# Performance work log

Measured on AMD Instinct MI355X. Metric: run time of the kernel, lower is better.

The kernel has to match this reference:

```python
import jax, jax.numpy as jnp
import numpy as np

B, N, C = 4, 4096, 128  # batch, tokens (flattened 3D volume), channels
F = 128  # filters


def setup_inputs() -> dict:
    key = jax.random.key(0)
    ks = jax.random.split(key, 7)
    s = 1.0 / np.sqrt(C)
    return {
        "inputs": jax.random.normal(ks[0], (B, N, C), dtype=jnp.float32),
        "Wq": jax.random.normal(ks[1], (C, F), dtype=jnp.float32) * s,
        "bq": jnp.zeros((F,), dtype=jnp.float32),
        "Wk": jax.random.normal(ks[2], (C, F), dtype=jnp.float32) * s,
        "bk": jnp.zeros((F,), dtype=jnp.float32),
        "Wv": jax.random.normal(ks[3], (C, F), dtype=jnp.float32) * s,
        "bv": jnp.zeros((F,), dtype=jnp.float32),
    }


def reference(inputs, Wq, bq, Wk, bk, Wv, bv):
    # Dense projections
    q = inputs @ Wq + bq  # [B, N, F]
    k = inputs @ Wk + bk
    v = inputs @ Wv + bv
    scale = jnp.sqrt(jnp.asarray(F, dtype=q.dtype))
    scores = jnp.einsum("bnf,bmf->bnm", q, k) / scale  # [B, N, N]
    weights = jax.nn.softmax(scores, axis=-1)
    return jnp.einsum("bnm,bmf->bnf", weights, v)
```

## Files before the change

### kernel.cpp

```cpp
#include <hip/hip_runtime.h>

typedef unsigned short u16;
typedef unsigned int u32;
typedef float f32x4 __attribute__((ext_vector_type(4)));
typedef short s16x8 __attribute__((ext_vector_type(8)));
typedef unsigned int u32x2 __attribute__((ext_vector_type(2)));
typedef unsigned int u32x4 __attribute__((ext_vector_type(4)));

#define NB 4
#define NT 4096
#define ND 128
#define NQ (NB * NT)

#define QK_SCALE 0.12751879523138906f

using as3_void = __attribute__((address_space(3))) void;
using as1_void = __attribute__((address_space(1))) void;

__device__ __forceinline__ u16 f2bf(float x){
  unsigned u = __float_as_uint(x);
  return (u16)((u + 0x7FFFu + ((u >> 16) & 1u)) >> 16);
}
__device__ __forceinline__ u32 cvtpk(float lo, float hi){
  u32 r; asm("v_cvt_pk_bf16_f32 %0, %1, %2" : "=v"(r) : "v"(lo), "v"(hi)); return r;
}
__device__ __forceinline__ f32x4 mfma16(s16x8 a, s16x8 b, f32x4 c){
  return __builtin_amdgcn_mfma_f32_16x16x32_bf16(a, b, c, 0, 0, 0);
}

__global__ void k_wprep(const float* __restrict__ Wq, const float* __restrict__ Wk,
                        const float* __restrict__ Wv, u16* __restrict__ WT){
  int mat = blockIdx.x >> 7;
  int f   = blockIdx.x & 127;
  const float* W = (mat == 0) ? Wq : (mat == 1) ? Wk : Wv;
  int c = threadIdx.x;
  WT[mat * 16384 + f * 128 + c] = f2bf(W[c * 128 + f]);
}

__global__ __launch_bounds__(256) void k_proj(
    const float* __restrict__ X, const u16* __restrict__ WT,
    const float* __restrict__ bq, const float* __restrict__ bk, const float* __restrict__ bv,
    u16* __restrict__ Qs, u16* __restrict__ Ks, u16* __restrict__ VTs)
{
  __shared__ u16 vt[128 * 64];
  const int lane = threadIdx.x & 63;
  const int w    = threadIdx.x >> 6;
  const int lm = lane & 15, lg = lane >> 4;
  const int L   = (blockIdx.x & 7) * 96 + (blockIdx.x >> 3);
  const int mat = L % 3;
  const int rb  = L / 3;
  const int rowbase = rb * 64 + w * 16;

  s16x8 a[4];
  const float* xr = X + (size_t)(rowbase + lm) * ND;
  #pragma unroll
  for (int kc = 0; kc < 4; ++kc){
    f32x4 x0 = *(const f32x4*)(xr + kc * 32 + lg * 8);
    f32x4 x1 = *(const f32x4*)(xr + kc * 32 + lg * 8 + 4);
    s16x8 t;
    t[0]=(short)f2bf(x0[0]); t[1]=(short)f2bf(x0[1]); t[2]=(short)f2bf(x0[2]); t[3]=(short)f2bf(x0[3]);
    t[4]=(short)f2bf(x1[0]); t[5]=(short)f2bf(x1[1]); t[6]=(short)f2bf(x1[2]); t[7]=(short)f2bf(x1[3]);
    a[kc] = t;
  }

  const float* bias = (mat == 0) ? bq : (mat == 1) ? bk : bv;
  float bl[8];
  #pragma unroll
  for (int n = 0; n < 8; ++n) bl[n] = bias[n * 16 + lm];
  f32x4 acc[8];
  #pragma unroll
  for (int n = 0; n < 8; ++n) acc[n] = f32x4{0.f,0.f,0.f,0.f};
  #pragma unroll
  for (int kc = 0; kc < 4; ++kc){
    #pragma unroll
    for (int n = 0; n < 8; ++n){
      s16x8 bf = *(const s16x8*)&WT[mat*16384 + (n*16 + lm)*128 + kc*32 + lg*8];
      acc[n] = mfma16(a[kc], bf, acc[n]);
    }
  }

  if (mat == 0){
    #pragma unroll
    for (int n = 0; n < 8; ++n){
      int f = n * 16 + lm;
      #pragma unroll
      for (int i = 0; i < 4; ++i){
        int r = rowbase + lg * 4 + i;
        Qs[(size_t)r * ND + f] = f2bf((acc[n][i] + bl[n]) * QK_SCALE);
      }
    }
  } else if (mat == 1){
    #pragma unroll
    for (int n = 0; n < 8; ++n){
      int f = n * 16 + lm;
      #pragma unroll
      for (int i = 0; i < 4; ++i){
        int r = rowbase + lg * 4 + i;
        Ks[(size_t)r * ND + (f ^ ((r & 7) << 3))] = f2bf(acc[n][i] + bl[n]);
      }
    }
  } else {
    #pragma unroll
    for (int n = 0; n < 8; ++n){
      int f = n * 16 + lm;
      #pragma unroll
      for (int i = 0; i < 4; ++i){
        int stcol = (w * 16 + lg * 4 + i) ^ ((f & 3) << 3) ^ (((f >> 2) & 1) << 2);
        vt[f * 64 + (stcol ^ ((f & 7) << 3))] = f2bf(acc[n][i] + bl[n]);
      }
    }
    __syncthreads();
    const int b2  = (rb * 64) >> 12;
    const int nt0 = (rb * 64) & (NT - 1);
    #pragma unroll
    for (int it = 0; it < 4; ++it){
      int c = it * 256 + threadIdx.x;
      int f = c >> 3, ch = c & 7;
      s16x8 v = *(const s16x8*)&vt[f * 64 + ((ch * 8) ^ ((f & 7) << 3))];
      *(s16x8*)&VTs[((size_t)b2 * ND + f) * NT + nt0 + ch * 8] = v;
    }
  }
}

__global__ __launch_bounds__(512, 4) void k_attn(
    const u16* __restrict__ Qs, const u16* __restrict__ Ks,
    const u16* __restrict__ VTs, u16* __restrict__ Op, float* __restrict__ lp)
{
  __shared__ __align__(16) u16 lds[32768];
  __shared__ float lbuf[4][32];
  u16* kbuf = lds;
  u16* vbuf = lds + 16384;

  const int lin = blockIdx.x;
  const int logical = (lin & 7) * 64 + (lin >> 3);
  const int qblk = logical & 127;
  const int quarter = logical >> 7;

  const int lane = threadIdx.x & 63;
  const int w  = threadIdx.x >> 6;
  const int qw = w >> 1, g = w & 1;
  const int lm = lane & 15, lg = lane >> 4;
  const int q0 = qblk * 128 + qw * 32;
  const int b  = q0 >> 12;
  const int kv0 = quarter * 1024 + g * 512;

  s16x8 aq[2][4];
  #pragma unroll
  for (int sq = 0; sq < 2; ++sq){
    const u16* qr = Qs + (size_t)(q0 + sq * 16 + lm) * ND;
    #pragma unroll
    for (int kc = 0; kc < 4; ++kc) aq[sq][kc] = *(const s16x8*)(qr + kc * 32 + lg * 8);
  }

  f32x4 o[2][8];
  #pragma unroll
  for (int sq = 0; sq < 2; ++sq)
    #pragma unroll
    for (int n = 0; n < 8; ++n) o[sq][n] = f32x4{0.f,0.f,0.f,0.f};
  float l_[2] = {0.f, 0.f};

  const u16* gk = Ks  + ((size_t)b * NT + kv0 + qw * 8 + (lane >> 4)) * ND + (lane & 15) * 8;
  const u16* gv = VTs + ((size_t)b * ND + qw * 32 + (lane >> 2)) * NT + kv0 + (lane & 3) * 8;

  auto stage = [&](int buf){
    u16* kd = kbuf + (buf * 2 + g) * 4096 + qw * 1024;
    u16* vd = vbuf + (buf * 2 + g) * 4096 + qw * 1024;
    __builtin_amdgcn_global_load_lds((const as1_void*)gk,
                                     (as3_void*)kd, 16, 0, 0);
    __builtin_amdgcn_global_load_lds((const as1_void*)(gk + (size_t)4 * ND),
                                     (as3_void*)(kd + 512), 16, 0, 0);
    __builtin_amdgcn_global_load_lds((const as1_void*)gv,
                                     (as3_void*)vd, 16, 0, 0);
    __builtin_amdgcn_global_load_lds((const as1_void*)(gv + (size_t)16 * NT),
                                     (as3_void*)(vd + 512), 16, 0, 0);
    gk += (size_t)32 * ND;
    gv += 32;
  };

  const int kswz = (lm & 7) << 3;
  const int vswz = ((lm & 3) << 3) ^ (((lm >> 2) & 1) << 2);
  const int vcol0 = (lg * 4) ^ vswz;
  const int vcol1 = (16 + lg * 4) ^ vswz;

  stage(0);
  __syncthreads();
  int par = 0;

  for (int t = 0; t < 16; ++t){
    if (t < 15) stage(par ^ 1);
    const u16* kb = kbuf + (par * 2 + g) * 4096;
    const u16* vb = vbuf + (par * 2 + g) * 4096;

    f32x4 st[2][2];
    #pragma unroll
    for (int sq = 0; sq < 2; ++sq)
      #pragma unroll
      for (int n = 0; n < 2; ++n) st[sq][n] = f32x4{0.f,0.f,0.f,0.f};
    __builtin_amdgcn_s_setprio(1);
    #pragma unroll
    for (int kc = 0; kc < 4; ++kc){
      #pragma unroll
      for (int n = 0; n < 2; ++n){
        s16x8 kf = *(const s16x8*)&kb[(n * 16 + lm) * 128 + ((kc * 32 + lg * 8) ^ kswz)];
        st[0][n] = mfma16(kf, aq[0][kc], st[0][n]);
        st[1][n] = mfma16(kf, aq[1][kc], st[1][n]);
      }
    }
    __builtin_amdgcn_s_setprio(0);

    s16x8 pa[2];
    #pragma unroll
    for (int sq = 0; sq < 2; ++sq){
      float p[8];
      #pragma unroll
      for (int n = 0; n < 2; ++n)
        #pragma unroll
        for (int i = 0; i < 4; ++i){
          p[n * 4 + i] = __builtin_amdgcn_exp2f(st[sq][n][i]);
          l_[sq] += p[n * 4 + i];
        }
      pa[sq] = __builtin_bit_cast(s16x8, u32x4{
          cvtpk(p[0], p[1]), cvtpk(p[2], p[3]),
          cvtpk(p[4], p[5]), cvtpk(p[6], p[7])});
    }

    __builtin_amdgcn_s_setprio(1);
    #pragma unroll
    for (int nf = 0; nf < 8; ++nf){
      const int vr = (nf * 16 + lm) * 32;
      u32x2 v0 = *(const u32x2*)&vb[vr + vcol0];
      u32x2 v1 = *(const u32x2*)&vb[vr + vcol1];
      s16x8 vf = __builtin_bit_cast(s16x8, u32x4{v0[0], v0[1], v1[0], v1[1]});
      o[0][nf] = mfma16(pa[0], vf, o[0][nf]);
      o[1][nf] = mfma16(pa[1], vf, o[1][nf]);
    }
    __builtin_amdgcn_s_setprio(0);

    __syncthreads();
    par ^= 1;
  }

  #pragma unroll
  for (int sq = 0; sq < 2; ++sq){
    float v = l_[sq];
    v += __shfl_xor(v, 16);
    v += __shfl_xor(v, 32);
    l_[sq] = v;
  }

  float* mbF = (float*)lds;
  __syncthreads();
  if (g == 1){
    #pragma unroll
    for (int sq = 0; sq < 2; ++sq){
      #pragma unroll
      for (int i = 0; i < 4; ++i)
        #pragma unroll
        for (int nf = 0; nf < 8; ++nf)
          mbF[qw * 4096 + (sq * 16 + lg * 4 + i) * 128 + nf * 16 + lm] = o[sq][nf][i];
      if (lg == 0) lbuf[qw][sq * 16 + lm] = l_[sq];
    }
  }
  __syncthreads();
  if (g == 0){
    #pragma unroll
    for (int sq = 0; sq < 2; ++sq){
      l_[sq] += lbuf[qw][sq * 16 + lm];
      #pragma unroll
      for (int i = 0; i < 4; ++i){
        const size_t r = (size_t)quarter * NQ + q0 + sq * 16 + lg * 4 + i;
        #pragma unroll
        for (int nf = 0; nf < 8; ++nf)
          Op[r * ND + nf * 16 + lm] = f2bf(
              o[sq][nf][i] + mbF[qw * 4096 + (sq * 16 + lg * 4 + i) * 128 + nf * 16 + lm]);
      }
      if (lg == 0) lp[(size_t)quarter * NQ + q0 + sq * 16 + lm] = l_[sq];
    }
  }
}

__global__ __launch_bounds__(256) void k_merge(const u16* __restrict__ Op,
                                               const float* __restrict__ lp,
                                               float* __restrict__ Out){
  const int gid = blockIdx.x * 256 + threadIdx.x;
  const int q = gid >> 4, c = gid & 15;
  const float inv = 1.f / (lp[q] + lp[NQ + q] + lp[2 * NQ + q] + lp[3 * NQ + q]);
  float acc[8] = {0,0,0,0,0,0,0,0};
  #pragma unroll
  for (int qt = 0; qt < 4; ++qt){
    s16x8 v = *(const s16x8*)(Op + ((size_t)qt * NQ + q) * ND + c * 8);
    #pragma unroll
    for (int j = 0; j < 8; ++j)
      acc[j] += __uint_as_float(((u32)(u16)v[j]) << 16);
  }
  f32x4 r0{acc[0]*inv, acc[1]*inv, acc[2]*inv, acc[3]*inv};
  f32x4 r1{acc[4]*inv, acc[5]*inv, acc[6]*inv, acc[7]*inv};
  *(f32x4*)(Out + (size_t)q * ND + c * 8)     = r0;
  *(f32x4*)(Out + (size_t)q * ND + c * 8 + 4) = r1;
}

extern "C" void kernel_launch(void* const* d_in, const int* in_sizes, int n_in,
                              void* d_out, int out_size, void* d_ws, size_t ws_size,
                              hipStream_t stream) {
  const float* X  = (const float*)d_in[0];
  const float* Wq = (const float*)d_in[1];
  const float* bq = (const float*)d_in[2];
  const float* Wk = (const float*)d_in[3];
  const float* bk = (const float*)d_in[4];
  const float* Wv = (const float*)d_in[5];
  const float* bv = (const float*)d_in[6];
  float* Out = (float*)d_out;

  u16* Qs  = (u16*)d_ws;
  u16* Ks  = Qs  + (size_t)NQ * ND;
  u16* VTs = Ks  + (size_t)NQ * ND;
  u16* WT  = VTs + (size_t)NQ * ND;
  u16* Op  = WT + 3 * 128 * 128;
  float* lp = (float*)(Op + (size_t)4 * NQ * ND);

  hipLaunchKernelGGL(k_wprep, dim3(3 * 128), dim3(128), 0, stream, Wq, Wk, Wv, WT);
  hipLaunchKernelGGL(k_proj,  dim3(768), dim3(256), 0, stream,
                     X, WT, bq, bk, bv, Qs, Ks, VTs);
  hipLaunchKernelGGL(k_attn,  dim3(512), dim3(512), 0, stream, Qs, Ks, VTs, Op, lp);
  hipLaunchKernelGGL(k_merge, dim3(NQ * 16 / 256), dim3(256), 0, stream, Op, lp, Out);
}
```

Before: 81.17 us.

## Fuse split-KV merge into attention kernel via last-block atomic counter

Removes the separate merge kernel launch. Each attention block increments a per-query-block atomic counter after writing its partial output, and the fourth block to finish reduces the four partials and writes the final normalized output. The block-to-work mapping is changed so the four KV quarters of a query block sit on the same XCD, which keeps their partials close in cache. This saves a kernel launch and the global round-trip, but leaves the merge work serialized on the tail blocks and adds a memset plus atomics.

```diff
diff --git a/kernel.cpp b/kernel.cpp
--- a/kernel.cpp
+++ b/kernel.cpp
@@ -124,17 +124,20 @@
 
 __global__ __launch_bounds__(512, 4) void k_attn(
     const u16* __restrict__ Qs, const u16* __restrict__ Ks,
-    const u16* __restrict__ VTs, u16* __restrict__ Op, float* __restrict__ lp)
+    const u16* __restrict__ VTs, u16* __restrict__ Op, float* __restrict__ lp,
+    int* __restrict__ cnt, float* __restrict__ Out)
 {
   __shared__ __align__(16) u16 lds[32768];
   __shared__ float lbuf[4][32];
+  __shared__ int lastflag;
   u16* kbuf = lds;
   u16* vbuf = lds + 16384;
 
   const int lin = blockIdx.x;
-  const int logical = (lin & 7) * 64 + (lin >> 3);
-  const int qblk = logical & 127;
-  const int quarter = logical >> 7;
+  const int xcd = lin & 7;
+  const int idx = lin >> 3;
+  const int qblk = xcd * 16 + (idx >> 2);
+  const int quarter = idx & 3;
 
   const int lane = threadIdx.x & 63;
   const int w  = threadIdx.x >> 6;
@@ -277,26 +280,38 @@
       if (lg == 0) lp[(size_t)quarter * NQ + q0 + sq * 16 + lm] = l_[sq];
     }
   }
-}
-
-__global__ __launch_bounds__(256) void k_merge(const u16* __restrict__ Op,
-                                               const float* __restrict__ lp,
-                                               float* __restrict__ Out){
-  const int gid = blockIdx.x * 256 + threadIdx.x;
-  const int q = gid >> 4, c = gid & 15;
-  const float inv = 1.f / (lp[q] + lp[NQ + q] + lp[2 * NQ + q] + lp[3 * NQ + q]);
-  float acc[8] = {0,0,0,0,0,0,0,0};
-  #pragma unroll
-  for (int qt = 0; qt < 4; ++qt){
-    s16x8 v = *(const s16x8*)(Op + ((size_t)qt * NQ + q) * ND + c * 8);
-    #pragma unroll
-    for (int j = 0; j < 8; ++j)
-      acc[j] += __uint_as_float(((u32)(u16)v[j]) << 16);
-  }
-  f32x4 r0{acc[0]*inv, acc[1]*inv, acc[2]*inv, acc[3]*inv};
-  f32x4 r1{acc[4]*inv, acc[5]*inv, acc[6]*inv, acc[7]*inv};
-  *(f32x4*)(Out + (size_t)q * ND + c * 8)     = r0;
-  *(f32x4*)(Out + (size_t)q * ND + c * 8 + 4) = r1;
+
+  __threadfence();
+  __syncthreads();
+  if (threadIdx.x == 0){
+    int old = __hip_atomic_fetch_add(&cnt[qblk], 1, __ATOMIC_ACQ_REL,
+                                     __HIP_MEMORY_SCOPE_AGENT);
+    lastflag = (old == 3);
+    if (old == 3) cnt[qblk] = 0;
+  }
+  __syncthreads();
+  if (lastflag){
+    __threadfence();
+    #pragma unroll
+    for (int it = 0; it < 4; ++it){
+      const int id  = it * 512 + threadIdx.x;
+      const int row = id >> 4, fc = id & 15;
+      const size_t q = (size_t)qblk * 128 + row;
+      const float inv = 1.f / (lp[q] + lp[NQ + q] + lp[2 * NQ + q] + lp[3 * NQ + q]);
+      float acc[8] = {0,0,0,0,0,0,0,0};
+      #pragma unroll
+      for (int qt = 0; qt < 4; ++qt){
+        s16x8 v = *(const s16x8*)(Op + ((size_t)qt * NQ + q) * ND + fc * 8);
+        #pragma unroll
+        for (int j = 0; j < 8; ++j)
+          acc[j] += __uint_as_float(((u32)(u16)v[j]) << 16);
+      }
+      f32x4 r0{acc[0]*inv, acc[1]*inv, acc[2]*inv, acc[3]*inv};
+      f32x4 r1{acc[4]*inv, acc[5]*inv, acc[6]*inv, acc[7]*inv};
+      *(f32x4*)(Out + q * ND + fc * 8)     = r0;
+      *(f32x4*)(Out + q * ND + fc * 8 + 4) = r1;
+    }
+  }
 }
 
 extern "C" void kernel_launch(void* const* d_in, const int* in_sizes, int n_in,
@@ -317,10 +332,12 @@
   u16* WT  = VTs + (size_t)NQ * ND;
   u16* Op  = WT + 3 * 128 * 128;
   float* lp = (float*)(Op + (size_t)4 * NQ * ND);
-
+  int* cnt  = (int*)(lp + (size_t)4 * NQ);
+
+  hipMemsetAsync(cnt, 0, 128 * sizeof(int), stream);
   hipLaunchKernelGGL(k_wprep, dim3(3 * 128), dim3(128), 0, stream, Wq, Wk, Wv, WT);
   hipLaunchKernelGGL(k_proj,  dim3(768), dim3(256), 0, stream,
                      X, WT, bq, bk, bv, Qs, Ks, VTs);
-  hipLaunchKernelGGL(k_attn,  dim3(512), dim3(512), 0, stream, Qs, Ks, VTs, Op, lp);
-  hipLaunchKernelGGL(k_merge, dim3(NQ * 16 / 256), dim3(256), 0, stream, Op, lp, Out);
-}
+  hipLaunchKernelGGL(k_attn,  dim3(512), dim3(512), 0, stream,
+                     Qs, Ks, VTs, Op, lp, cnt, Out);
+}
```

New measurement: 248.3 us. 3.06x slower.

## Split attention KV into eighths across blocks instead of intra-block wave pairs

Applied to the files above, without the earlier changes.

The attention kernel drops the two-wave-group intra-block KV split and its LDS-based partial reduction. Instead it launches twice as many 256-thread blocks, each covering one eighth of the keys, and writes eight partial outputs. The merge kernel now sums eight partials. This removes the in-block reduction and barriers and halves LDS per block, which could raise occupancy. In exchange it doubles partial-output traffic through global memory in bf16 and makes the merge kernel's work larger.

```diff
diff --git a/kernel.cpp b/kernel.cpp
--- a/kernel.cpp
+++ b/kernel.cpp
@@ -122,27 +122,23 @@
   }
 }
 
-__global__ __launch_bounds__(512, 4) void k_attn(
+__global__ __launch_bounds__(256, 4) void k_attn(
     const u16* __restrict__ Qs, const u16* __restrict__ Ks,
     const u16* __restrict__ VTs, u16* __restrict__ Op, float* __restrict__ lp)
 {
-  __shared__ __align__(16) u16 lds[32768];
-  __shared__ float lbuf[4][32];
-  u16* kbuf = lds;
-  u16* vbuf = lds + 16384;
+  __shared__ __align__(16) u16 kbuf[2][32 * 128];
+  __shared__ __align__(16) u16 vbuf[2][128 * 32];
 
   const int lin = blockIdx.x;
-  const int logical = (lin & 7) * 64 + (lin >> 3);
-  const int qblk = logical & 127;
-  const int quarter = logical >> 7;
+  const int qblk   = (lin & 7) * 16 + (lin >> 6);
+  const int eighth = (lin >> 3) & 7;
 
   const int lane = threadIdx.x & 63;
-  const int w  = threadIdx.x >> 6;
-  const int qw = w >> 1, g = w & 1;
+  const int qw = threadIdx.x >> 6;
   const int lm = lane & 15, lg = lane >> 4;
   const int q0 = qblk * 128 + qw * 32;
   const int b  = q0 >> 12;
-  const int kv0 = quarter * 1024 + g * 512;
+  const int kv0 = eighth * 512;
 
   s16x8 aq[2][4];
   #pragma unroll
@@ -163,8 +159,8 @@
   const u16* gv = VTs + ((size_t)b * ND + qw * 32 + (lane >> 2)) * NT + kv0 + (lane & 3) * 8;
 
   auto stage = [&](int buf){
-    u16* kd = kbuf + (buf * 2 + g) * 4096 + qw * 1024;
-    u16* vd = vbuf + (buf * 2 + g) * 4096 + qw * 1024;
+    u16* kd = &kbuf[buf][qw * 1024];
+    u16* vd = &vbuf[buf][qw * 1024];
     __builtin_amdgcn_global_load_lds((const as1_void*)gk,
                                      (as3_void*)kd, 16, 0, 0);
     __builtin_amdgcn_global_load_lds((const as1_void*)(gk + (size_t)4 * ND),
@@ -188,8 +184,8 @@
 
   for (int t = 0; t < 16; ++t){
     if (t < 15) stage(par ^ 1);
-    const u16* kb = kbuf + (par * 2 + g) * 4096;
-    const u16* vb = vbuf + (par * 2 + g) * 4096;
+    const u16* kb = &kbuf[par][0];
+    const u16* vb = &vbuf[par][0];
 
     f32x4 st[2][2];
     #pragma unroll
@@ -247,35 +243,16 @@
     v += __shfl_xor(v, 32);
     l_[sq] = v;
   }
-
-  float* mbF = (float*)lds;
-  __syncthreads();
-  if (g == 1){
-    #pragma unroll
-    for (int sq = 0; sq < 2; ++sq){
-      #pragma unroll
-      for (int i = 0; i < 4; ++i)
-        #pragma unroll
-        for (int nf = 0; nf < 8; ++nf)
-          mbF[qw * 4096 + (sq * 16 + lg * 4 + i) * 128 + nf * 16 + lm] = o[sq][nf][i];
-      if (lg == 0) lbuf[qw][sq * 16 + lm] = l_[sq];
-    }
-  }
-  __syncthreads();
-  if (g == 0){
-    #pragma unroll
-    for (int sq = 0; sq < 2; ++sq){
-      l_[sq] += lbuf[qw][sq * 16 + lm];
-      #pragma unroll
-      for (int i = 0; i < 4; ++i){
-        const size_t r = (size_t)quarter * NQ + q0 + sq * 16 + lg * 4 + i;
-        #pragma unroll
-        for (int nf = 0; nf < 8; ++nf)
-          Op[r * ND + nf * 16 + lm] = f2bf(
-              o[sq][nf][i] + mbF[qw * 4096 + (sq * 16 + lg * 4 + i) * 128 + nf * 16 + lm]);
-      }
-      if (lg == 0) lp[(size_t)quarter * NQ + q0 + sq * 16 + lm] = l_[sq];
-    }
+  #pragma unroll
+  for (int sq = 0; sq < 2; ++sq){
+    #pragma unroll
+    for (int i = 0; i < 4; ++i){
+      const size_t r = (size_t)eighth * NQ + q0 + sq * 16 + lg * 4 + i;
+      #pragma unroll
+      for (int nf = 0; nf < 8; ++nf)
+        Op[r * ND + nf * 16 + lm] = f2bf(o[sq][nf][i]);
+    }
+    if (lg == 0) lp[(size_t)eighth * NQ + q0 + sq * 16 + lm] = l_[sq];
   }
 }
 
@@ -284,11 +261,14 @@
                                                float* __restrict__ Out){
   const int gid = blockIdx.x * 256 + threadIdx.x;
   const int q = gid >> 4, c = gid & 15;
-  const float inv = 1.f / (lp[q] + lp[NQ + q] + lp[2 * NQ + q] + lp[3 * NQ + q]);
+  float lsum = 0.f;
+  #pragma unroll
+  for (int e = 0; e < 8; ++e) lsum += lp[(size_t)e * NQ + q];
+  const float inv = 1.f / lsum;
   float acc[8] = {0,0,0,0,0,0,0,0};
   #pragma unroll
-  for (int qt = 0; qt < 4; ++qt){
-    s16x8 v = *(const s16x8*)(Op + ((size_t)qt * NQ + q) * ND + c * 8);
+  for (int e = 0; e < 8; ++e){
+    s16x8 v = *(const s16x8*)(Op + ((size_t)e * NQ + q) * ND + c * 8);
     #pragma unroll
     for (int j = 0; j < 8; ++j)
       acc[j] += __uint_as_float(((u32)(u16)v[j]) << 16);
@@ -316,11 +296,11 @@
   u16* VTs = Ks  + (size_t)NQ * ND;
   u16* WT  = VTs + (size_t)NQ * ND;
   u16* Op  = WT + 3 * 128 * 128;
-  float* lp = (float*)(Op + (size_t)4 * NQ * ND);
+  float* lp = (float*)(Op + (size_t)8 * NQ * ND);
 
   hipLaunchKernelGGL(k_wprep, dim3(3 * 128), dim3(128), 0, stream, Wq, Wk, Wv, WT);
   hipLaunchKernelGGL(k_proj,  dim3(768), dim3(256), 0, stream,
                      X, WT, bq, bk, bv, Qs, Ks, VTs);
-  hipLaunchKernelGGL(k_attn,  dim3(512), dim3(512), 0, stream, Qs, Ks, VTs, Op, lp);
+  hipLaunchKernelGGL(k_attn,  dim3(1024), dim3(256), 0, stream, Qs, Ks, VTs, Op, lp);
   hipLaunchKernelGGL(k_merge, dim3(NQ * 16 / 256), dim3(256), 0, stream, Op, lp, Out);
 }
```

Result: no change. 81.87 us (+0.9%).
